# Performance work log

Hardware: AMD Instinct MI355X
Metric: run time of the kernel (lower is better)

Reference implementation:

```python
import jax, jax.numpy as jnp
import numpy as np
from jax import lax

B, N, E, CIN, COUT, H, W, KS = 32, 32, 128, 64, 128, 128, 128, 3


def setup_inputs() -> dict:
    key = jax.random.key(0)
    ks = jax.random.split(key, 12)
    xav = lambda k, shape: jax.random.normal(k, shape, jnp.float32) * np.sqrt(2.0 / (shape[0] + shape[1]))
    return {
        "game_board": jax.random.randint(ks[0], (B, H, W), 0, N, jnp.int32),
        "state": jax.random.normal(ks[1], (B, CIN, H, W), jnp.float32),
        "node_embeds": jax.random.normal(ks[2], (N, E), jnp.float32),
        "goal_embed": jax.random.normal(ks[3], (B, E), jnp.float32),
        "char_to_node": jnp.arange(N, dtype=jnp.int32),
        "conv_w": jax.random.normal(ks[4], (COUT, CIN, KS, KS), jnp.float32) * np.sqrt(1.0 / (CIN * KS * KS)),
        "conv_b": jnp.zeros((COUT,), jnp.float32),
        "wQ": xav(ks[5], (2 * E, E)),
        "wK": xav(ks[6], (2 * E, E)),
        "wV": xav(ks[7], (2 * E, E)),
        "final_w": xav(ks[8], (COUT, E)),  # torch Linear weight [out, in]
        "final_b": jnp.zeros((COUT,), jnp.float32),
    }


def reference(game_board, state, node_embeds, goal_embed, char_to_node,
              conv_w, conv_b, wQ, wK, wV, final_w, final_b):
    # Conv2d, stride 1, padding kernel//2 -> same spatial size. [B,COUT,H,W]
    pad = KS // 2
    conv_out = lax.conv_general_dilated(
        state, conv_w, (1, 1), [(pad, pad), (pad, pad)],
        dimension_numbers=("NCHW", "OIHW", "NCHW")) + conv_b[None, :, None, None]

    # Node attention: cat(node, goal) along feature dim -> [B,N,2E]
    node_b = jnp.broadcast_to(node_embeds[None], (B, N, E))
    goal_b = jnp.broadcast_to(goal_embed[:, None, :], (B, N, E))
    x = jnp.concatenate([node_b, goal_b], axis=-1)  # [B,N,2E]
    Q = jnp.einsum("bnf,fk->bnk", x, wQ)
    K = jnp.einsum("bnf,fk->bnk", x, wK)
    V = jnp.einsum("bnf,fk->bnk", x, wV)
    scores = jnp.einsum("bqk,bnk->bqn", Q, K) / np.sqrt(float(E))
    atten = jnp.einsum("bqn,bnk->bqk", jax.nn.softmax(scores, axis=-1), V)  # [B,N,E]
    out_node = jnp.einsum("bnk,ok->bno", atten, final_w) + final_b  # [B,N,COUT]

    # embed_state: place node embedding at every grid cell whose char maps to that node.
    # char_to_node is the inverse of node_2_game_char (identity here); one gather per cell.
    node_idx = char_to_node[game_board]  # [B,H,W]
    gathered = jnp.take_along_axis(
        out_node, node_idx.reshape(B, H * W, 1), axis=1).reshape(B, H, W, COUT)
    valid = ((game_board >= 0) & (game_board < N)).astype(gathered.dtype)[..., None]
    out = conv_out.transpose(0, 2, 3, 1) + gathered * valid  # [B,H,W,COUT]
    return out.transpose(0, 3, 1, 2)  # [B,COUT,H,W]
```

## Files before the change

kernel.cpp:

```cpp
#include <hip/hip_runtime.h>
#include <hip/hip_bf16.h>

#define B_    32
#define N_    32
#define E_    128
#define CIN_  64
#define COUT_ 128
#define H_    128
#define W_    128

using bf16x8 = __attribute__((ext_vector_type(8))) short;
using sh4    = __attribute__((ext_vector_type(4))) short;
using f32x4  = __attribute__((ext_vector_type(4))) float;

static __device__ __forceinline__ unsigned short f2bf(float f) {
  union { float f; unsigned u; } v; v.f = f;
  unsigned r = v.u + 0x7FFFu + ((v.u >> 16) & 1u);
  return (unsigned short)(r >> 16);
}

__global__ void pack_w_kernel(const float* __restrict__ conv_w, short* __restrict__ Wp) {
  int idx = blockIdx.x * 256 + threadIdx.x;
  if (idx >= COUT_ * CIN_ * 9) return;
  int cout = idx / (CIN_ * 9);
  int rem  = idx % (CIN_ * 9);
  int ci   = rem / 9;
  int tap  = rem % 9;
  Wp[(tap * COUT_ + cout) * CIN_ + ci] = (short)f2bf(conv_w[idx]);
}

__global__ void qkv_kernel(const float* __restrict__ node_embeds,
                           const float* __restrict__ goal_embed,
                           const float* __restrict__ wQ,
                           const float* __restrict__ wK,
                           const float* __restrict__ wV,
                           float* __restrict__ qkv) {
  __shared__ float x[32][260];
  int tid = threadIdx.x;
  int kg = blockIdx.x, mat = blockIdx.y, b = blockIdx.z;
  const float* W = (mat == 0) ? wQ : (mat == 1) ? wK : wV;
  for (int e = tid; e < 4096; e += 256) x[e >> 7][e & 127] = node_embeds[e];
  for (int e = tid; e < 4096; e += 256) x[e >> 7][128 + (e & 127)] = goal_embed[b * 128 + (e & 127)];
  __syncthreads();
  int k  = kg * 16 + (tid & 15);
  int n0 = tid >> 4, n1 = n0 + 16;
  float a0 = 0.f, a1 = 0.f;
  for (int f = 0; f < 256; f += 4) {
    float4 xv0 = *(const float4*)&x[n0][f];
    float4 xv1 = *(const float4*)&x[n1][f];
    float w0 = W[(f + 0) * 128 + k];
    float w1 = W[(f + 1) * 128 + k];
    float w2 = W[(f + 2) * 128 + k];
    float w3 = W[(f + 3) * 128 + k];
    a0 += xv0.x * w0 + xv0.y * w1 + xv0.z * w2 + xv0.w * w3;
    a1 += xv1.x * w0 + xv1.y * w1 + xv1.z * w2 + xv1.w * w3;
  }
  int base = (mat * 32 + b) * 32;
  qkv[(base + n0) * 128 + k] = a0;
  qkv[(base + n1) * 128 + k] = a1;
}

__global__ void attn_kernel(const float* __restrict__ qkv, float* __restrict__ atten) {
  __shared__ float QS[32][132], KS[32][132], VS[32][132];
  __shared__ float S[32][33];
  int tid = threadIdx.x, b = blockIdx.x;
  const float* q0 = qkv + b * 4096;
  const float* k0 = qkv + 131072 + b * 4096;
  const float* v0 = qkv + 262144 + b * 4096;
  for (int e = tid; e < 4096; e += 256) {
    int n = e >> 7, k = e & 127;
    QS[n][k] = q0[e]; KS[n][k] = k0[e]; VS[n][k] = v0[e];
  }
  __syncthreads();
  for (int p = tid; p < 1024; p += 256) {
    int qi = p >> 5, ni = p & 31;
    float acc = 0.f;
    for (int k = 0; k < 128; k += 4) {
      float4 a = *(const float4*)&QS[qi][k];
      float4 c = *(const float4*)&KS[ni][k];
      acc += a.x * c.x + a.y * c.y + a.z * c.z + a.w * c.w;
    }
    S[qi][ni] = acc * 0.08838834764831845f;
  }
  __syncthreads();
  if (tid < 32) {
    float mx = -1e30f;
    for (int n = 0; n < 32; ++n) mx = fmaxf(mx, S[tid][n]);
    float sum = 0.f;
    for (int n = 0; n < 32; ++n) { float e = __expf(S[tid][n] - mx); S[tid][n] = e; sum += e; }
    float inv = 1.f / sum;
    for (int n = 0; n < 32; ++n) S[tid][n] *= inv;
  }
  __syncthreads();
  int qi = tid >> 3, ks = (tid & 7) * 16;
  float4 A0 = {0,0,0,0}, A1 = {0,0,0,0}, A2 = {0,0,0,0}, A3 = {0,0,0,0};
  for (int n = 0; n < 32; ++n) {
    float p = S[qi][n];
    float4 v_0 = *(const float4*)&VS[n][ks];
    float4 v_1 = *(const float4*)&VS[n][ks + 4];
    float4 v_2 = *(const float4*)&VS[n][ks + 8];
    float4 v_3 = *(const float4*)&VS[n][ks + 12];
    A0.x += p * v_0.x; A0.y += p * v_0.y; A0.z += p * v_0.z; A0.w += p * v_0.w;
    A1.x += p * v_1.x; A1.y += p * v_1.y; A1.z += p * v_1.z; A1.w += p * v_1.w;
    A2.x += p * v_2.x; A2.y += p * v_2.y; A2.z += p * v_2.z; A2.w += p * v_2.w;
    A3.x += p * v_3.x; A3.y += p * v_3.y; A3.z += p * v_3.z; A3.w += p * v_3.w;
  }
  float* op = atten + (b * 32 + qi) * 128 + ks;
  *(float4*)&op[0] = A0; *(float4*)&op[4] = A1; *(float4*)&op[8] = A2; *(float4*)&op[12] = A3;
}

__global__ void final_kernel(const float* __restrict__ atten, const float* __restrict__ fw,
                             const float* __restrict__ fb, float* __restrict__ out_node) {
  __shared__ float ar[128];
  int tid = threadIdx.x;
  int n = blockIdx.x, b = blockIdx.y;
  ar[tid] = atten[(b * 32 + n) * 128 + tid];
  __syncthreads();
  const float* fr = fw + tid * 128;
  float acc = fb[tid];
  for (int k = 0; k < 128; k += 4) {
    float4 f = *(const float4*)&fr[k];
    acc += ar[k] * f.x + ar[k + 1] * f.y + ar[k + 2] * f.z + ar[k + 3] * f.w;
  }
  out_node[(b * 32 + n) * 128 + tid] = acc;
}

#define CIP 68
#define TLX 66
__global__ __launch_bounds__(256) void conv_kernel(
    const float* __restrict__ state, const float* __restrict__ conv_b,
    const int* __restrict__ game_board, const int* __restrict__ char_to_node,
    const short* __restrict__ Wp, const float* __restrict__ out_node,
    float* __restrict__ out) {
  __shared__ short tile[4 * TLX * CIP];
  int tid = threadIdx.x;
  int lane = tid & 63, wave = tid >> 6;
  int y0 = blockIdx.x * 2;
  int x0 = blockIdx.y * 64;
  int b  = blockIdx.z;

  for (int task = wave; task < 128; task += 4) {
    int cp = task >> 2;
    int yy = task & 3;
    int gy = y0 - 1 + yy;
    const float* srow = state + ((b * 64 + 2 * cp) * 128 + gy) * 128;
    {
      int xt = lane, gx = x0 - 1 + xt;
      float v0 = 0.f, v1 = 0.f;
      if (gy >= 0 && gy < 128 && gx >= 0 && gx < 128) { v0 = srow[gx]; v1 = srow[16384 + gx]; }
      unsigned pk = (unsigned)f2bf(v0) | ((unsigned)f2bf(v1) << 16);
      *(unsigned*)&tile[(yy * TLX + xt) * CIP + 2 * cp] = pk;
    }
    if (lane < 2) {
      int xt = 64 + lane, gx = x0 - 1 + xt;
      float v0 = 0.f, v1 = 0.f;
      if (gy >= 0 && gy < 128 && gx >= 0 && gx < 128) { v0 = srow[gx]; v1 = srow[16384 + gx]; }
      unsigned pk = (unsigned)f2bf(v0) | ((unsigned)f2bf(v1) << 16);
      *(unsigned*)&tile[(yy * TLX + xt) * CIP + 2 * cp] = pk;
    }
  }
  __syncthreads();

  int q = lane >> 4, i = lane & 15;
  int mtset = (wave >> 1) * 4;
  int ty    = wave & 1;

  f32x4 acc[4][4];
#pragma unroll
  for (int m = 0; m < 4; ++m)
#pragma unroll
    for (int n = 0; n < 4; ++n) acc[m][n] = (f32x4){0.f, 0.f, 0.f, 0.f};

  const short* wbase = Wp + i * 64 + q * 8;
  bf16x8 aF[4];
#pragma unroll
  for (int m = 0; m < 4; ++m) aF[m] = *(const bf16x8*)(wbase + (mtset + m) * 1024);

  int base_cell = (ty * TLX + i) * CIP + q * 8;

  for (int chunk = 0; chunk < 18; ++chunk) {
    int t = chunk >> 1, h = chunk & 1;
    int kh = t / 3, kw = t - kh * 3;
    int off = (kh * TLX + kw) * CIP + h * 32;
    bf16x8 bF[4];
#pragma unroll
    for (int ntl = 0; ntl < 4; ++ntl) {
      const short* p = tile + base_cell + ntl * (16 * CIP) + off;
      sh4 lo = *(const sh4*)(p);
      sh4 hi = *(const sh4*)(p + 4);
      bF[ntl] = __builtin_shufflevector(lo, hi, 0, 1, 2, 3, 4, 5, 6, 7);
    }
    bf16x8 aN[4];
    if (chunk < 17) {
      int c2 = chunk + 1;
      const short* wb2 = wbase + (c2 >> 1) * 8192 + (c2 & 1) * 32;
#pragma unroll
      for (int m = 0; m < 4; ++m) aN[m] = *(const bf16x8*)(wb2 + (mtset + m) * 1024);
    }
#pragma unroll
    for (int m = 0; m < 4; ++m)
#pragma unroll
      for (int n = 0; n < 4; ++n)
        acc[m][n] = __builtin_amdgcn_mfma_f32_16x16x32_bf16(aF[m], bF[n], acc[m][n], 0, 0, 0);
    if (chunk < 17) {
#pragma unroll
      for (int m = 0; m < 4; ++m) aF[m] = aN[m];
    }
  }

  int gy = y0 + ty;
#pragma unroll
  for (int ntl = 0; ntl < 4; ++ntl) {
    int gx = x0 + ntl * 16 + i;
    int gb = game_board[(b * 128 + gy) * 128 + gx];
    bool valid = (gb >= 0 && gb < 32);
    int nidx = 0;
    if (valid) { nidx = char_to_node[gb]; nidx = nidx < 0 ? 0 : (nidx > 31 ? 31 : nidx); }
    const float* gn = out_node + (b * 32 + nidx) * 128;
#pragma unroll
    for (int m = 0; m < 4; ++m) {
      int c0 = (mtset + m) * 16 + q * 4;
      float4 bias = *(const float4*)(conv_b + c0);
      float4 g = valid ? *(const float4*)(gn + c0) : make_float4(0.f, 0.f, 0.f, 0.f);
      f32x4 a = acc[m][ntl];
      int obase = (b * 128 + c0) * 16384 + gy * 128 + gx;
      out[obase]         = a[0] + bias.x + g.x;
      out[obase + 16384] = a[1] + bias.y + g.y;
      out[obase + 32768] = a[2] + bias.z + g.z;
      out[obase + 49152] = a[3] + bias.w + g.w;
    }
  }
}

extern "C" void kernel_launch(void* const* d_in, const int* in_sizes, int n_in,
                              void* d_out, int out_size, void* d_ws, size_t ws_size,
                              hipStream_t stream) {
  const int*   game_board   = (const int*)  d_in[0];
  const float* state        = (const float*)d_in[1];
  const float* node_embeds  = (const float*)d_in[2];
  const float* goal_embed   = (const float*)d_in[3];
  const int*   char_to_node = (const int*)  d_in[4];
  const float* conv_w       = (const float*)d_in[5];
  const float* conv_b       = (const float*)d_in[6];
  const float* wQ           = (const float*)d_in[7];
  const float* wK           = (const float*)d_in[8];
  const float* wV           = (const float*)d_in[9];
  const float* final_w      = (const float*)d_in[10];
  const float* final_b      = (const float*)d_in[11];
  float* out = (float*)d_out;

  char* ws = (char*)d_ws;
  short* Wp       = (short*)(ws);
  float* qkv      = (float*)(ws + 147456);
  float* atten    = (float*)(ws + 1720320);
  float* out_node = (float*)(ws + 2244608);

  hipLaunchKernelGGL(pack_w_kernel, dim3(288), dim3(256), 0, stream, conv_w, Wp);
  hipLaunchKernelGGL(qkv_kernel, dim3(8, 3, 32), dim3(256), 0, stream,
                     node_embeds, goal_embed, wQ, wK, wV, qkv);
  hipLaunchKernelGGL(attn_kernel, dim3(32), dim3(256), 0, stream, qkv, atten);
  hipLaunchKernelGGL(final_kernel, dim3(32, 32), dim3(128), 0, stream, atten, final_w, final_b, out_node);
  hipLaunchKernelGGL(conv_kernel, dim3(64, 2, 32), dim3(256), 0, stream,
                     state, conv_b, game_board, char_to_node, Wp, out_node, out);
}
```

Measured before the change: 733.4 us.

## Pre-pack state into padded swizzled NHWC bf16 and stage conv tiles via direct LDS loads

```diff
diff --git a/kernel.cpp b/kernel.cpp
--- a/kernel.cpp
+++ b/kernel.cpp
@@ -10,7 +10,6 @@
 #define W_    128
 
 using bf16x8 = __attribute__((ext_vector_type(8))) short;
-using sh4    = __attribute__((ext_vector_type(4))) short;
 using f32x4  = __attribute__((ext_vector_type(4))) float;
 
 static __device__ __forceinline__ unsigned short f2bf(float f) {
@@ -19,45 +18,91 @@
   return (unsigned short)(r >> 16);
 }
 
-__global__ void pack_w_kernel(const float* __restrict__ conv_w, short* __restrict__ Wp) {
-  int idx = blockIdx.x * 256 + threadIdx.x;
-  if (idx >= COUT_ * CIN_ * 9) return;
-  int cout = idx / (CIN_ * 9);
-  int rem  = idx % (CIN_ * 9);
-  int ci   = rem / 9;
-  int tap  = rem % 9;
-  Wp[(tap * COUT_ + cout) * CIN_ + ci] = (short)f2bf(conv_w[idx]);
-}
-
-__global__ void qkv_kernel(const float* __restrict__ node_embeds,
-                           const float* __restrict__ goal_embed,
-                           const float* __restrict__ wQ,
-                           const float* __restrict__ wK,
-                           const float* __restrict__ wV,
-                           float* __restrict__ qkv) {
-  __shared__ float x[32][260];
-  int tid = threadIdx.x;
-  int kg = blockIdx.x, mat = blockIdx.y, b = blockIdx.z;
-  const float* W = (mat == 0) ? wQ : (mat == 1) ? wK : wV;
-  for (int e = tid; e < 4096; e += 256) x[e >> 7][e & 127] = node_embeds[e];
-  for (int e = tid; e < 4096; e += 256) x[e >> 7][128 + (e & 127)] = goal_embed[b * 128 + (e & 127)];
-  __syncthreads();
-  int k  = kg * 16 + (tid & 15);
-  int n0 = tid >> 4, n1 = n0 + 16;
-  float a0 = 0.f, a1 = 0.f;
-  for (int f = 0; f < 256; f += 4) {
-    float4 xv0 = *(const float4*)&x[n0][f];
-    float4 xv1 = *(const float4*)&x[n1][f];
-    float w0 = W[(f + 0) * 128 + k];
-    float w1 = W[(f + 1) * 128 + k];
-    float w2 = W[(f + 2) * 128 + k];
-    float w3 = W[(f + 3) * 128 + k];
-    a0 += xv0.x * w0 + xv0.y * w1 + xv0.z * w2 + xv0.w * w3;
-    a1 += xv1.x * w0 + xv1.y * w1 + xv1.z * w2 + xv1.w * w3;
-  }
-  int base = (mat * 32 + b) * 32;
-  qkv[(base + n0) * 128 + k] = a0;
-  qkv[(base + n1) * 128 + k] = a1;
+static __device__ __forceinline__ void gl2lds16(const void* g, void* l) {
+  __builtin_amdgcn_global_load_lds(
+      (const __attribute__((address_space(1))) unsigned int*)g,
+      (__attribute__((address_space(3))) unsigned int*)l, 16, 0, 0);
+}
+
+__global__ __launch_bounds__(256) void prep_kernel(
+    const float* __restrict__ state, const float* __restrict__ node_embeds,
+    const float* __restrict__ goal_embed, const float* __restrict__ conv_w,
+    const float* __restrict__ wQ, const float* __restrict__ wK,
+    const float* __restrict__ wV,
+    short* __restrict__ nhwc, short* __restrict__ Wp, float* __restrict__ qkv) {
+  __shared__ __align__(16) unsigned char smem[33280];
+  int bid = blockIdx.x, tid = threadIdx.x;
+
+  if (bid < 4096) {
+    int b = bid >> 7, y = bid & 127;
+    unsigned* lds = (unsigned*)smem;
+    int cp = tid >> 3;
+    int xo = (tid & 7) << 4;
+    const float* r0 = state + (((b * 64 + 2 * cp) * 128 + y) * 128) + xo;
+    const float* r1 = r0 + 16384;
+    float4 a0[4], a1[4];
+#pragma unroll
+    for (int j = 0; j < 4; ++j) { a0[j] = *(const float4*)(r0 + 4 * j); a1[j] = *(const float4*)(r1 + 4 * j); }
+    int k16 = cp >> 2;
+    const float* f0 = (const float*)a0;
+    const float* f1 = (const float*)a1;
+#pragma unroll
+    for (int jj = 0; jj < 16; ++jj) {
+      int x = xo + jj;
+      unsigned pk = (unsigned)f2bf(f0[jj]) | ((unsigned)f2bf(f1[jj]) << 16);
+      lds[x * 32 + (((k16 + x + 1) & 7) << 2) + (cp & 3)] = pk;
+    }
+    __syncthreads();
+    int cell = tid >> 1, h = tid & 1;
+    unsigned* rowbase = (unsigned*)nhwc + (size_t)((b * 130 + y + 1) * 136) * 32;
+    unsigned* dst = rowbase + (cell + 1) * 32 + h * 16;
+    unsigned* src = lds + cell * 32 + h * 16;
+#pragma unroll
+    for (int k = 0; k < 4; ++k) *(uint4*)(dst + 4 * k) = *(uint4*)(src + 4 * k);
+    if (tid < 32) rowbase[tid] = 0;
+    else rowbase[129 * 32 + (tid - 32)] = 0;
+  } else if (bid < 4160) {
+    int idx = bid - 4096;
+    int b = idx >> 1, yp = (idx & 1) ? 129 : 0;
+    unsigned* rowbase = (unsigned*)nhwc + (size_t)((b * 130 + yp) * 136) * 32;
+    for (int k = tid; k < 136 * 32; k += 256) rowbase[k] = 0;
+  } else if (bid < 4448) {
+    int idx = (bid - 4160) * 256 + tid;
+    if (idx < COUT_ * CIN_ * 9) {
+      int cout = idx / (CIN_ * 9);
+      int rem  = idx % (CIN_ * 9);
+      int ci   = rem / 9;
+      int tap  = rem % 9;
+      Wp[(tap * COUT_ + cout) * CIN_ + ci] = (short)f2bf(conv_w[idx]);
+    }
+  } else {
+    int idx = bid - 4448;
+    int kg = idx & 7;
+    int r  = idx >> 3;
+    int b  = r / 3;
+    int mat = r - b * 3;
+    const float* W = (mat == 0) ? wQ : (mat == 1) ? wK : wV;
+    float (*x)[260] = (float(*)[260])smem;
+    for (int e = tid; e < 4096; e += 256) x[e >> 7][e & 127] = node_embeds[e];
+    for (int e = tid; e < 4096; e += 256) x[e >> 7][128 + (e & 127)] = goal_embed[b * 128 + (e & 127)];
+    __syncthreads();
+    int k  = kg * 16 + (tid & 15);
+    int n0 = tid >> 4, n1 = n0 + 16;
+    float a0 = 0.f, a1 = 0.f;
+    for (int f = 0; f < 256; f += 4) {
+      float4 xv0 = *(const float4*)&x[n0][f];
+      float4 xv1 = *(const float4*)&x[n1][f];
+      float w0 = W[(f + 0) * 128 + k];
+      float w1 = W[(f + 1) * 128 + k];
+      float w2 = W[(f + 2) * 128 + k];
+      float w3 = W[(f + 3) * 128 + k];
+      a0 += xv0.x * w0 + xv0.y * w1 + xv0.z * w2 + xv0.w * w3;
+      a1 += xv1.x * w0 + xv1.y * w1 + xv1.z * w2 + xv1.w * w3;
+    }
+    int base = (mat * 32 + b) * 32;
+    qkv[(base + n0) * 128 + k] = a0;
+    qkv[(base + n1) * 128 + k] = a1;
+  }
 }
 
 __global__ void attn_kernel(const float* __restrict__ qkv, float* __restrict__ atten) {
@@ -125,39 +170,25 @@
   out_node[(b * 32 + n) * 128 + tid] = acc;
 }
 
-#define CIP 68
-#define TLX 66
+#define XC 72
 __global__ __launch_bounds__(256) void conv_kernel(
-    const float* __restrict__ state, const float* __restrict__ conv_b,
+    const short* __restrict__ nhwc, const float* __restrict__ conv_b,
     const int* __restrict__ game_board, const int* __restrict__ char_to_node,
     const short* __restrict__ Wp, const float* __restrict__ out_node,
     float* __restrict__ out) {
-  __shared__ short tile[4 * TLX * CIP];
+  __shared__ __align__(16) short tile[4 * XC * 64];
   int tid = threadIdx.x;
   int lane = tid & 63, wave = tid >> 6;
   int y0 = blockIdx.x * 2;
   int x0 = blockIdx.y * 64;
   int b  = blockIdx.z;
 
-  for (int task = wave; task < 128; task += 4) {
-    int cp = task >> 2;
-    int yy = task & 3;
-    int gy = y0 - 1 + yy;
-    const float* srow = state + ((b * 64 + 2 * cp) * 128 + gy) * 128;
-    {
-      int xt = lane, gx = x0 - 1 + xt;
-      float v0 = 0.f, v1 = 0.f;
-      if (gy >= 0 && gy < 128 && gx >= 0 && gx < 128) { v0 = srow[gx]; v1 = srow[16384 + gx]; }
-      unsigned pk = (unsigned)f2bf(v0) | ((unsigned)f2bf(v1) << 16);
-      *(unsigned*)&tile[(yy * TLX + xt) * CIP + 2 * cp] = pk;
-    }
-    if (lane < 2) {
-      int xt = 64 + lane, gx = x0 - 1 + xt;
-      float v0 = 0.f, v1 = 0.f;
-      if (gy >= 0 && gy < 128 && gx >= 0 && gx < 128) { v0 = srow[gx]; v1 = srow[16384 + gx]; }
-      unsigned pk = (unsigned)f2bf(v0) | ((unsigned)f2bf(v1) << 16);
-      *(unsigned*)&tile[(yy * TLX + xt) * CIP + 2 * cp] = pk;
-    }
+  {
+    const short* grow = nhwc + (size_t)((b * 130 + y0 + wave) * 136 + x0) * 64;
+    short* lrow = tile + wave * (XC * 64);
+#pragma unroll
+    for (int ch = 0; ch < 9; ++ch)
+      gl2lds16(grow + ch * 512 + lane * 8, lrow + ch * 512 + lane * 8);
   }
   __syncthreads();
 
@@ -176,19 +207,15 @@
 #pragma unroll
   for (int m = 0; m < 4; ++m) aF[m] = *(const bf16x8*)(wbase + (mtset + m) * 1024);
 
-  int base_cell = (ty * TLX + i) * CIP + q * 8;
-
   for (int chunk = 0; chunk < 18; ++chunk) {
     int t = chunk >> 1, h = chunk & 1;
     int kh = t / 3, kw = t - kh * 3;
-    int off = (kh * TLX + kw) * CIP + h * 32;
+    int row = ty + kh;
     bf16x8 bF[4];
 #pragma unroll
     for (int ntl = 0; ntl < 4; ++ntl) {
-      const short* p = tile + base_cell + ntl * (16 * CIP) + off;
-      sh4 lo = *(const sh4*)(p);
-      sh4 hi = *(const sh4*)(p + 4);
-      bF[ntl] = __builtin_shufflevector(lo, hi, 0, 1, 2, 3, 4, 5, 6, 7);
+      int c = ntl * 16 + i + kw;
+      bF[ntl] = *(const bf16x8*)(tile + (row * XC + c) * 64 + (((h * 4 + q + c) & 7) << 3));
     }
     bf16x8 aN[4];
     if (chunk < 17) {
@@ -254,12 +281,12 @@
   float* qkv      = (float*)(ws + 147456);
   float* atten    = (float*)(ws + 1720320);
   float* out_node = (float*)(ws + 2244608);
-
-  hipLaunchKernelGGL(pack_w_kernel, dim3(288), dim3(256), 0, stream, conv_w, Wp);
-  hipLaunchKernelGGL(qkv_kernel, dim3(8, 3, 32), dim3(256), 0, stream,
-                     node_embeds, goal_embed, wQ, wK, wV, qkv);
+  short* nhwc     = (short*)(ws + 2768896);
+
+  hipLaunchKernelGGL(prep_kernel, dim3(5216), dim3(256), 0, stream,
+                     state, node_embeds, goal_embed, conv_w, wQ, wK, wV, nhwc, Wp, qkv);
   hipLaunchKernelGGL(attn_kernel, dim3(32), dim3(256), 0, stream, qkv, atten);
   hipLaunchKernelGGL(final_kernel, dim3(32, 32), dim3(128), 0, stream, atten, final_w, final_b, out_node);
   hipLaunchKernelGGL(conv_kernel, dim3(64, 2, 32), dim3(256), 0, stream,
-                     state, conv_b, game_board, char_to_node, Wp, out_node, out);
-}
+                     nhwc, conv_b, game_board, char_to_node, Wp, out_node, out);
+}
```

Result: faster. 618.2 us (-15.7%).
